# Kernel tuning notes

Hardware: AMD Instinct MI355X
Metric: run time of the kernel (lower is better)

The kernel has to match this reference:

```python
import jax, jax.numpy as jnp
import numpy as np

WS = 8           # window size
NUM_HEADS = 16
DIM = 512
HEAD_DIM = DIM // NUM_HEADS


def _relative_position_index(ws):
    coords = np.stack(np.meshgrid(np.arange(ws), np.arange(ws), indexing='ij'))  # (2, ws, ws)
    cf = coords.reshape(2, -1)                                   # (2, ws*ws)
    rel = cf[:, :, None] - cf[:, None, :]                        # (2, N, N)
    rel = rel.transpose(1, 2, 0).copy()
    rel[:, :, 0] += ws - 1
    rel[:, :, 1] += ws - 1
    rel[:, :, 0] *= 2 * ws - 1
    return jnp.asarray(rel.sum(-1))                              # (N, N) int


REL_IDX = _relative_position_index(WS)


def setup_inputs() -> dict:
    key = jax.random.key(0)
    ks = jax.random.split(key, 4)
    B, C, H, W = 4, DIM, 128, 128
    x = jax.random.normal(ks[0], (B, C, H, W), dtype=jnp.float32)
    gamma = jnp.ones((DIM,), jnp.float32)
    beta = jnp.zeros((DIM,), jnp.float32)
    w_qkv = jax.random.normal(ks[1], (DIM, 3 * DIM), jnp.float32) * (DIM ** -0.5)
    w_proj = jax.random.normal(ks[2], (DIM, DIM), jnp.float32) * (DIM ** -0.5)
    b_proj = jnp.zeros((DIM,), jnp.float32)
    bias_table = jax.random.normal(ks[3], ((2 * WS - 1) ** 2, NUM_HEADS), jnp.float32) * 0.02
    return {"x": x, "gamma": gamma, "beta": beta, "w_qkv": w_qkv,
            "w_proj": w_proj, "b_proj": b_proj, "bias_table": bias_table}


def reference(x, gamma, beta, w_qkv, w_proj, b_proj, bias_table):
    B, C, H, W = x.shape
    pad_h = (WS - H % WS) % WS
    pad_w = (WS - W % WS) % WS
    x = jnp.pad(x, ((0, 0), (0, 0), (0, pad_h), (0, pad_w)))
    Hp, Wp = H + pad_h, W + pad_w
    nh, nw = Hp // WS, Wp // WS
    N = WS * WS  # tokens per window

    # window partition: (B,C,Hp,Wp) -> (B*nh*nw, N, C)
    xw = x.reshape(B, C, nh, WS, nw, WS).transpose(0, 2, 4, 3, 5, 1)
    xw = xw.reshape(B * nh * nw, N, C)

    # LayerNorm over channels
    mu = jnp.mean(xw, axis=-1, keepdims=True)
    var = jnp.var(xw, axis=-1, keepdims=True)
    xn = (xw - mu) * jax.lax.rsqrt(var + 1e-5) * gamma + beta

    # QKV projection (no bias)
    qkv = (xn @ w_qkv).reshape(-1, N, 3, NUM_HEADS, HEAD_DIM)
    qkv = qkv.transpose(2, 0, 3, 1, 4)   # (3, nWin, heads, N, hd)
    q, k, v = qkv[0], qkv[1], qkv[2]

    scale = HEAD_DIM ** -0.5
    attn = jnp.einsum('whnd,whmd->whnm', q, k) * scale          # (nWin, heads, N, N)
    rel_bias = bias_table[REL_IDX]                               # (N, N, heads)
    attn = attn + rel_bias.transpose(2, 0, 1)[None]
    attn = jax.nn.softmax(attn, axis=-1)

    out = jnp.einsum('whnm,whmd->wnhd', attn, v).reshape(-1, N, C)
    out = out @ w_proj + b_proj

    # un-window: (B*nh*nw, N, C) -> (B, C, Hp, Wp)
    out = out.reshape(B, nh, nw, WS, WS, C).transpose(0, 5, 1, 3, 2, 4)
    out = out.reshape(B, C, Hp, Wp)
    return out[:, :, :H, :W]
```

## Files before the change

### kernel.cpp

```cpp
#include <hip/hip_runtime.h>

typedef unsigned short u16;
typedef unsigned int u32;
typedef unsigned long long u64;
typedef __bf16 bf16x8 __attribute__((ext_vector_type(8)));
typedef float f32x4 __attribute__((ext_vector_type(4)));

#define C_DIM 512
#define QKV_N 1536
#define KDIM 512
#define NHEAD 16
#define HD 32
#define H_IMG 128
#define W_IMG 128
#define HW 16384
#define NTOK 65536
#define NWIN 1024

#define GLL(g, l) __builtin_amdgcn_global_load_lds( \
    (const __attribute__((address_space(1))) u32*)(g), \
    (__attribute__((address_space(3))) u32*)(l), 16, 0, 0)

#define BAR() __builtin_amdgcn_s_barrier()
#define LGKM0() asm volatile("s_waitcnt lgkmcnt(0)" ::: "memory")
#define VM6() asm volatile("s_waitcnt vmcnt(6)" ::: "memory")
#define VM0() asm volatile("s_waitcnt vmcnt(0)" ::: "memory")

__device__ __forceinline__ u16 f2bf(float f) {
    u32 u = __builtin_bit_cast(u32, f);
    u += 0x7fffu + ((u >> 16) & 1u);
    return (u16)(u >> 16);
}
__device__ __forceinline__ float bf2f(u16 v) {
    return __builtin_bit_cast(float, (u32)v << 16);
}

__global__ void sa_prep_kernel(const float* __restrict__ w_qkv,
                               const float* __restrict__ w_proj,
                               const float* __restrict__ bias_table,
                               u16* __restrict__ wqT, u16* __restrict__ wpT,
                               u16* __restrict__ biasP) {
    int t = blockIdx.x * 256 + threadIdx.x;
    const int W1 = KDIM * QKV_N;
    const int W2 = KDIM * C_DIM;
    const int W3 = NHEAD * 64 * 64;
    if (t < W1) {
        int k = t / QKV_N, n = t % QKV_N;
        wqT[n * KDIM + k] = f2bf(w_qkv[t]);
    } else if (t < W1 + W2) {
        int u = t - W1;
        int k = u / C_DIM, n = u % C_DIM;
        wpT[n * KDIM + k] = f2bf(w_proj[u]);
    } else if (t < W1 + W2 + W3) {
        int u = t - W1 - W2;
        int h = u >> 12, n = (u >> 6) & 63, m = u & 63;
        int di = (n >> 3) - (m >> 3) + 7;
        int dj = (n & 7) - (m & 7) + 7;
        biasP[(h << 12) + (n << 6) + ((m & 15) << 2) + (m >> 4)] =
            f2bf(bias_table[(di * 15 + dj) * NHEAD + h]);
    }
}

__global__ __launch_bounds__(512, 4) void sa_ln_fused_kernel(const float* __restrict__ x,
        const float* __restrict__ gamma, const float* __restrict__ beta,
        u16* __restrict__ xnc) {
    __shared__ u16 tile[64 * 513];
    __shared__ float psum[8][64], psq[8][64];
    __shared__ float smu[64], srs[64];
    int bid = blockIdx.x;
    int win = (bid & 7) * (NWIN / 8) + (bid >> 3);
    int b = win >> 8, wl = win & 255;
    int wh = wl >> 4, ww = wl & 15;
    int tid = threadIdx.x;
    int lane = tid & 63, wv = tid >> 6;
    int cph = tid >> 4;
    int r = (tid >> 1) & 7, q = tid & 1;
    int nbase = r * 8 + q * 4;
    const float* xb = x + (size_t)b * C_DIM * HW
                        + (size_t)(wh * 8 + r) * W_IMG + ww * 8 + q * 4;
    float s[4] = {0.f, 0.f, 0.f, 0.f}, sq2[4] = {0.f, 0.f, 0.f, 0.f};
#pragma unroll
    for (int it = 0; it < 16; ++it) {
        int c = cph + it * 32;
        float4 v = *reinterpret_cast<const float4*>(xb + (size_t)c * HW);
        float vv[4] = {v.x, v.y, v.z, v.w};
#pragma unroll
        for (int e = 0; e < 4; ++e) {
            _Float16 hv = (_Float16)vv[e];
            tile[(nbase + e) * 513 + c] = __builtin_bit_cast(u16, hv);
            s[e] += vv[e]; sq2[e] += vv[e] * vv[e];
        }
    }
#pragma unroll
    for (int e = 0; e < 4; ++e) {
        s[e]   += __shfl_xor(s[e],   16, 64);  s[e]   += __shfl_xor(s[e],   32, 64);
        sq2[e] += __shfl_xor(sq2[e], 16, 64);  sq2[e] += __shfl_xor(sq2[e], 32, 64);
    }
    if ((lane >> 4) == 0) {
#pragma unroll
        for (int e = 0; e < 4; ++e) { psum[wv][nbase + e] = s[e]; psq[wv][nbase + e] = sq2[e]; }
    }
    __syncthreads();
    if (tid < 64) {
        float S = 0.f, Q = 0.f;
#pragma unroll
        for (int k = 0; k < 8; ++k) { S += psum[k][tid]; Q += psq[k][tid]; }
        float m = S * (1.f / C_DIM);
        float var = Q * (1.f / C_DIM) - m * m;
        smu[tid] = m; srs[tid] = rsqrtf(var + 1e-5f);
    }
    __syncthreads();
    int n = tid & 63;
    int gq = tid >> 6;
    float gg[8], bb[8];
#pragma unroll
    for (int c0 = 0; c0 < 8; ++c0) { gg[c0] = gamma[c0 * 64 + n]; bb[c0] = beta[c0 * 64 + n]; }
#pragma unroll
    for (int it = 0; it < 8; ++it) {
        int nn = it * 8 + gq;
        float m = smu[nn], rs = srs[nn];
        u16* op = xnc + (size_t)((win << 6) + nn) * C_DIM;
#pragma unroll
        for (int c0 = 0; c0 < 8; ++c0) {
            int c = c0 * 64 + n;
            float v = (float)__builtin_bit_cast(_Float16, tile[nn * 513 + c]);
            op[c] = f2bf((v - m) * rs * gg[c0] + bb[c0]);
        }
    }
}


#define LDA1(Q,J,KK,BUF) af[Q][J][KK] = *reinterpret_cast<const bf16x8*>( \
    &lds[(BUF)*16384 + (wr*128 + ((Q)*2+(J))*16 + lr)*64 + ((((KK)*4)+lg) ^ (lr & 7))*8])
#define LDAQ(Q,BUF) do{ LDA1(Q,0,0,BUF); LDA1(Q,0,1,BUF); LDA1(Q,1,0,BUF); LDA1(Q,1,1,BUF); }while(0)
#define LDB1(NF,KK,BUF) bfr[NF][KK] = *reinterpret_cast<const bf16x8*>( \
    &lds[32768 + (BUF)*16384 + (wc*64 + (NF)*16 + lr)*64 + ((((KK)*4)+lg) ^ (lr & 7))*8])
#define LDB(BUF) do{ LDB1(0,0,BUF); LDB1(0,1,BUF); LDB1(1,0,BUF); LDB1(1,1,BUF); \
                     LDB1(2,0,BUF); LDB1(2,1,BUF); LDB1(3,0,BUF); LDB1(3,1,BUF); }while(0)
#define MFMA1(M,N,KK) acc[M][N] = __builtin_amdgcn_mfma_f32_16x16x32_bf16(af[(M)/2][(M)&1][KK], bfr[N][KK], acc[M][N], 0, 0, 0)
#define MFMAQ(Q) do{ __builtin_amdgcn_s_setprio(1); \
    MFMA1(2*(Q),0,0);   MFMA1(2*(Q),0,1);   MFMA1(2*(Q),1,0);   MFMA1(2*(Q),1,1); \
    MFMA1(2*(Q),2,0);   MFMA1(2*(Q),2,1);   MFMA1(2*(Q),3,0);   MFMA1(2*(Q),3,1); \
    MFMA1(2*(Q)+1,0,0); MFMA1(2*(Q)+1,0,1); MFMA1(2*(Q)+1,1,0); MFMA1(2*(Q)+1,1,1); \
    MFMA1(2*(Q)+1,2,0); MFMA1(2*(Q)+1,2,1); MFMA1(2*(Q)+1,3,0); MFMA1(2*(Q)+1,3,1); \
    __builtin_amdgcn_s_setprio(0); }while(0)
#define STAGE_A(SRC, KT, H) do{ const u16* _s = (SRC) + (KT)*64 + (size_t)((H)*128)*KDIM; \
    u16* _d = Adst + ((KT)&1)*16384 + (H)*8192; \
    GLL(_s, _d); GLL(_s + (size_t)64*KDIM, _d + 4096); }while(0)
#define STAGE_B(SRC, KT, H) do{ const u16* _s = (SRC) + (KT)*64 + (size_t)((H)*128)*KDIM; \
    u16* _d = Bdst + ((KT)&1)*16384 + (H)*8192; \
    GLL(_s, _d); GLL(_s + (size_t)64*KDIM, _d + 4096); }while(0)

template <int EPI>
__device__ __forceinline__ void gemm8_body(const u16* __restrict__ A,
        const u16* __restrict__ BT, u16* __restrict__ outB, u16* __restrict__ vT,
        float* __restrict__ outF, const float* __restrict__ bias,
        int nbx, int NT, u16* lds, int nblk) {
    const int tid = threadIdx.x;
    const int lane = tid & 63, wv = tid >> 6;
    const int wr = wv >> 2, wc = wv & 3;
    const int lr = lane & 15, lg = lane >> 4;
    const int arow = tid >> 3;
    const int axs = ((tid & 7) ^ ((tid >> 3) & 7)) * 8;
    u16* Adst = lds + tid * 8;
    u16* Bdst = lds + 32768 + tid * 8;

    const int cpx = nblk >> 3;
    const int t = ((int)blockIdx.x & 7) * cpx + ((int)blockIdx.x >> 3);
    const int mb = t / nbx, nb = t % nbx;
    const int m0 = mb * 256, n0 = nb * 256;
    const u16* Asrc = A  + (size_t)(m0 + arow) * KDIM + axs;
    const u16* Bsrc = BT + (size_t)(n0 + arow) * KDIM + axs;

    bf16x8 af[4][2][2];
    bf16x8 bfr[4][2];

    STAGE_A(Asrc, 0, 0); STAGE_A(Asrc, 0, 1); STAGE_B(Bsrc, 0, 0); STAGE_B(Bsrc, 0, 1);
    STAGE_B(Bsrc, 1, 0); STAGE_B(Bsrc, 1, 1); STAGE_A(Asrc, 1, 0);
    VM6(); BAR();

    f32x4 acc[8][4];
#pragma unroll
    for (int i = 0; i < 8; ++i)
#pragma unroll
        for (int j = 0; j < 4; ++j) acc[i][j] = {0.f, 0.f, 0.f, 0.f};

#pragma unroll 1
    for (int i = 0; i < 3; ++i) {
        LDB(0); LDAQ(0, 0); STAGE_A(Asrc, 2*i + 1, 1);
        BAR(); LGKM0(); MFMAQ(0); BAR();
        LDAQ(1, 0); LDAQ(2, 0); STAGE_B(Bsrc, 2*i + 2, 0);
        BAR(); LGKM0(); MFMAQ(1); BAR();
        LDAQ(3, 0); STAGE_B(Bsrc, 2*i + 2, 1);
        BAR(); LGKM0(); MFMAQ(2); BAR();
        STAGE_A(Asrc, 2*i + 2, 0);
        BAR(); LGKM0(); MFMAQ(3); VM6(); BAR();
        LDB(1); LDAQ(0, 1); STAGE_A(Asrc, 2*i + 2, 1);
        BAR(); LGKM0(); MFMAQ(0); BAR();
        LDAQ(1, 1); LDAQ(2, 1); STAGE_B(Bsrc, 2*i + 3, 0);
        BAR(); LGKM0(); MFMAQ(1); BAR();
        LDAQ(3, 1); STAGE_B(Bsrc, 2*i + 3, 1);
        BAR(); LGKM0(); MFMAQ(2); BAR();
        STAGE_A(Asrc, 2*i + 3, 0);
        BAR(); LGKM0(); MFMAQ(3); VM6(); BAR();
    }
    LDB(0); LDAQ(0, 0); STAGE_A(Asrc, 7, 1);
    BAR(); LGKM0(); MFMAQ(0); BAR();
    LDAQ(1, 0); LDAQ(2, 0);
    BAR(); LGKM0(); MFMAQ(1); BAR();
    LDAQ(3, 0);
    BAR(); LGKM0(); MFMAQ(2); BAR();
    BAR(); LGKM0(); MFMAQ(3); VM0(); BAR();
    LDB(1); LDAQ(0, 1);
    BAR(); LGKM0(); MFMAQ(0); BAR();
    LDAQ(1, 1); LDAQ(2, 1);
    BAR(); LGKM0(); MFMAQ(1); BAR();
    LDAQ(3, 1);
    BAR(); LGKM0(); MFMAQ(2); BAR();
    BAR(); LGKM0(); MFMAQ(3);

    if (EPI == 0) {
        if (n0 < 1024) {
#pragma unroll
            for (int mf = 0; mf < 8; ++mf) {
#pragma unroll
                for (int nf = 0; nf < 4; ++nf) {
                    int col = n0 + wc * 64 + nf * 16 + lr;
                    int row = m0 + wr * 128 + mf * 16 + lg * 4;
#pragma unroll
                    for (int rr = 0; rr < 4; ++rr)
                        outB[(size_t)(row + rr) * NT + col] = f2bf(acc[mf][nf][rr]);
                }
            }
        } else {
            __syncthreads();
#pragma unroll
            for (int mf = 0; mf < 8; ++mf) {
                int row = wr * 128 + mf * 16 + lg * 4;
#pragma unroll
                for (int nf = 0; nf < 4; ++nf) {
                    int col = wc * 64 + nf * 16 + lr;
                    u64 pk = (u64)f2bf(acc[mf][nf][0])
                           | ((u64)f2bf(acc[mf][nf][1]) << 16)
                           | ((u64)f2bf(acc[mf][nf][2]) << 32)
                           | ((u64)f2bf(acc[mf][nf][3]) << 48);
                    *reinterpret_cast<u64*>(&lds[col * 256 + (row ^ ((col & 7) << 3))]) = pk;
                }
            }
            __syncthreads();
            int win0 = m0 >> 6;
#pragma unroll
            for (int j = 0; j < 16; ++j) {
                int flat = j * 512 + tid;
                int col = flat >> 5, tokc = flat & 31;
                bf16x8 v = *reinterpret_cast<const bf16x8*>(
                    &lds[col * 256 + ((tokc * 8) ^ ((col & 7) << 3))]);
                int dg = (n0 - 1024) + col;
                int head = dg >> 5, d = dg & 31;
                int win = win0 + (tokc >> 3), tok = (tokc & 7) * 8;
                *reinterpret_cast<bf16x8*>(
                    &vT[(((size_t)win * NHEAD + head) * HD + d) * 64 + tok]) = v;
            }
        }
    } else {
        int win0 = m0 >> 6;
        int b_img = win0 >> 8, wl = win0 & 255;
        int h0 = (wl >> 4) * 8, w0 = (wl & 15) * 8;
        float* fbuf = reinterpret_cast<float*>(lds);
        __syncthreads();
#pragma unroll
        for (int s = 0; s < 2; ++s) {
            if ((wc >> 1) == s) {
                int half = wc & 1;
                float* cb = fbuf + half * 16384;
#pragma unroll
                for (int mf = 0; mf < 8; ++mf) {
#pragma unroll
                    for (int nf = 0; nf < 4; ++nf) {
                        int cp = nf * 16 + lr;
                        int row = wr * 128 + mf * 16 + lg * 4;
                        int h = (row >> 3) & 7;
                        int sl = ((row >> 6) & 3) * 2 + ((row >> 2) & 1);
                        float bbv = bias[n0 + (2 * s + half) * 64 + cp];
                        f32x4 v = acc[mf][nf];
                        float4 o = {v[0] + bbv, v[1] + bbv, v[2] + bbv, v[3] + bbv};
                        *reinterpret_cast<float4*>(&cb[cp * 256 + h * 32 + (sl ^ (cp & 7)) * 4]) = o;
                    }
                }
            }
            __syncthreads();
#pragma unroll
            for (int j = 0; j < 16; ++j) {
                int flat = j * 512 + tid;
                int half = flat >> 12, f = flat & 4095;
                int cp = f >> 6, h = (f >> 3) & 7, sl = f & 7;
                int col = n0 + (2 * s + half) * 64 + cp;
                float4 v = *reinterpret_cast<const float4*>(
                    &fbuf[half * 16384 + cp * 256 + h * 32 + ((sl ^ (cp & 7))) * 4]);
                *reinterpret_cast<float4*>(outF + (size_t)(b_img * C_DIM + col) * HW
                                           + (size_t)(h0 + h) * W_IMG + w0 + sl * 4) = v;
            }
            __syncthreads();
        }
    }
}

__global__ __launch_bounds__(512, 2) void sa_qkv_gemm(const u16* __restrict__ A,
        const u16* __restrict__ BT, u16* __restrict__ outB, u16* __restrict__ vT) {
    __shared__ u16 lds[65536];
    gemm8_body<0>(A, BT, outB, vT, nullptr, nullptr, 6, QKV_N, lds, 1536);
}

__global__ __launch_bounds__(512, 2) void sa_proj_gemm(const u16* __restrict__ A,
        const u16* __restrict__ BT, float* __restrict__ outF, const float* __restrict__ bias) {
    __shared__ u16 lds[65536];
    gemm8_body<1>(A, BT, nullptr, nullptr, outF, bias, 2, C_DIM, lds, 512);
}

__global__ __launch_bounds__(64) void sa_attn_kernel(const u16* __restrict__ qkv,
        const u16* __restrict__ vT, const u16* __restrict__ biasP, u16* __restrict__ attnc) {
    __shared__ u16 Ps[64 * 72];
    int bid = blockIdx.x;
    int win  = (bid & 7) * 128 + (bid >> 7);
    int head = (bid >> 3) & 15;
    int lane = threadIdx.x, lr = lane & 15, lg = lane >> 4;
    const u16* base = qkv + (size_t)win * 64 * QKV_N + head * HD;

    bf16x8 qa[4], kb[4];
#pragma unroll
    for (int mt = 0; mt < 4; ++mt)
        qa[mt] = *reinterpret_cast<const bf16x8*>(base + (size_t)(mt * 16 + lr) * QKV_N + lg * 8);
#pragma unroll
    for (int nt = 0; nt < 4; ++nt)
        kb[nt] = *reinterpret_cast<const bf16x8*>(base + (size_t)(nt * 16 + lr) * QKV_N + 512 + lg * 8);

    f32x4 sacc[4][4];
#pragma unroll
    for (int i = 0; i < 4; ++i)
#pragma unroll
        for (int j = 0; j < 4; ++j) sacc[i][j] = {0.f, 0.f, 0.f, 0.f};
#pragma unroll
    for (int mt = 0; mt < 4; ++mt)
#pragma unroll
        for (int nt = 0; nt < 4; ++nt)
            sacc[mt][nt] = __builtin_amdgcn_mfma_f32_16x16x32_bf16(qa[mt], kb[nt], sacc[mt][nt], 0, 0, 0);

    const u16* vbase = vT + ((size_t)win * NHEAD + head) * (HD * 64);
    bf16x8 vb[2][2];
#pragma unroll
    for (int ks = 0; ks < 2; ++ks)
#pragma unroll
        for (int n2 = 0; n2 < 2; ++n2)
            vb[ks][n2] = *reinterpret_cast<const bf16x8*>(
                &vbase[(n2 * 16 + lr) * 64 + ks * 32 + lg * 8]);

    const float scale = 0.17677669529663687f;
    const u16* bp = biasP + head * 4096;
#pragma unroll
    for (int mt = 0; mt < 4; ++mt) {
#pragma unroll
        for (int rr = 0; rr < 4; ++rr) {
            int row = mt * 16 + lg * 4 + rr;
            u64 braw = *reinterpret_cast<const u64*>(&bp[row * 64 + lr * 4]);
            float vals[4];
#pragma unroll
            for (int nt = 0; nt < 4; ++nt)
                vals[nt] = sacc[mt][nt][rr] * scale + bf2f((u16)(braw >> (16 * nt)));
            float mx = fmaxf(fmaxf(vals[0], vals[1]), fmaxf(vals[2], vals[3]));
#pragma unroll
            for (int d = 1; d < 16; d <<= 1) mx = fmaxf(mx, __shfl_xor(mx, d, 64));
            float sm = 0.f;
#pragma unroll
            for (int nt = 0; nt < 4; ++nt) { vals[nt] = __expf(vals[nt] - mx); sm += vals[nt]; }
#pragma unroll
            for (int d = 1; d < 16; d <<= 1) sm += __shfl_xor(sm, d, 64);
            float inv = 1.f / sm;
#pragma unroll
            for (int nt = 0; nt < 4; ++nt)
                Ps[row * 72 + nt * 16 + lr] = f2bf(vals[nt] * inv);
        }
    }
    __syncthreads();

    f32x4 oacc[4][2];
#pragma unroll
    for (int i = 0; i < 4; ++i) { oacc[i][0] = {0.f,0.f,0.f,0.f}; oacc[i][1] = {0.f,0.f,0.f,0.f}; }
#pragma unroll
    for (int ks = 0; ks < 2; ++ks) {
        bf16x8 pa[4];
#pragma unroll
        for (int mt = 0; mt < 4; ++mt)
            pa[mt] = *reinterpret_cast<const bf16x8*>(&Ps[(mt * 16 + lr) * 72 + ks * 32 + lg * 8]);
#pragma unroll
        for (int mt = 0; mt < 4; ++mt)
#pragma unroll
            for (int n2 = 0; n2 < 2; ++n2)
                oacc[mt][n2] = __builtin_amdgcn_mfma_f32_16x16x32_bf16(pa[mt], vb[ks][n2], oacc[mt][n2], 0, 0, 0);
    }

    __syncthreads();
    u16* o_lds = Ps;
#pragma unroll
    for (int mt = 0; mt < 4; ++mt)
#pragma unroll
        for (int n2 = 0; n2 < 2; ++n2)
#pragma unroll
            for (int rr = 0; rr < 4; ++rr) {
                int row = mt * 16 + lg * 4 + rr;
                o_lds[row * 40 + n2 * 16 + lr] = f2bf(oacc[mt][n2][rr]);
            }
    __syncthreads();
    u16* ob = attnc + (size_t)win * 64 * C_DIM + head * HD;
#pragma unroll
    for (int it2 = 0; it2 < 4; ++it2) {
        int flat = it2 * 64 + lane;
        int row = flat >> 2, ch = flat & 3;
        bf16x8 v = *reinterpret_cast<const bf16x8*>(&o_lds[row * 40 + ch * 8]);
        *reinterpret_cast<bf16x8*>(&ob[(size_t)row * C_DIM + ch * 8]) = v;
    }
}

extern "C" void kernel_launch(void* const* d_in, const int* in_sizes, int n_in,
                              void* d_out, int out_size, void* d_ws, size_t ws_size,
                              hipStream_t stream) {
    const float* x          = (const float*)d_in[0];
    const float* gamma      = (const float*)d_in[1];
    const float* beta       = (const float*)d_in[2];
    const float* w_qkv      = (const float*)d_in[3];
    const float* w_proj     = (const float*)d_in[4];
    const float* b_proj     = (const float*)d_in[5];
    const float* bias_table = (const float*)d_in[6];
    float* out = (float*)d_out;

    char* ws = (char*)d_ws;
    size_t off = 0;
    auto alloc = [&](size_t bytes) {
        char* p = ws + off;
        off += (bytes + 255) & ~(size_t)255;
        return p;
    };
    u16*   wqT   = (u16*)alloc((size_t)KDIM * QKV_N * 2);
    u16*   wpT   = (u16*)alloc((size_t)KDIM * C_DIM * 2);
    u16*   biasP = (u16*)alloc((size_t)NHEAD * 64 * 64 * 2);
    u16*   xnc   = (u16*)alloc((size_t)NTOK * C_DIM * 2);
    u16*   qkvc  = (u16*)alloc((size_t)NTOK * QKV_N * 2);
    u16*   vT    = (u16*)alloc((size_t)NWIN * NHEAD * HD * 64 * 2);
    u16*   attnc = (u16*)alloc((size_t)NTOK * C_DIM * 2);

    sa_prep_kernel<<<4352, 256, 0, stream>>>(w_qkv, w_proj, bias_table, wqT, wpT, biasP);
    sa_ln_fused_kernel<<<NWIN, 512, 0, stream>>>(x, gamma, beta, xnc);
    sa_qkv_gemm<<<1536, 512, 0, stream>>>(xnc, wqT, qkvc, vT);
    sa_attn_kernel<<<NWIN * NHEAD, 64, 0, stream>>>(qkvc, vT, biasP, attnc);
    sa_proj_gemm<<<512, 512, 0, stream>>>(attnc, wpT, out, b_proj);
}
```

Measured before the change: 306.9 us.

## Fuse window attention with output projection and vectorize LayerNorm stores

Merges the per-(window,head) attention kernel and the separate projection GEMM into one kernel per window. Eight waves each handle two heads and write attention outputs into LDS, then the block does the 64x512x512 projection reading wpT directly from global and stores NCHW fp32 output. This removes the attnc intermediate round-trip and one launch. In exchange, each block rereads the full projection weight from global/L2 without LDS staging and runs a smaller, less-tiled GEMM. Separately, the LayerNorm write-back now emits 16-byte vector stores per lane with a padded tile stride.

```diff
diff --git a/kernel.cpp b/kernel.cpp
--- a/kernel.cpp
+++ b/kernel.cpp
@@ -64,7 +64,7 @@
 __global__ __launch_bounds__(512, 4) void sa_ln_fused_kernel(const float* __restrict__ x,
         const float* __restrict__ gamma, const float* __restrict__ beta,
         u16* __restrict__ xnc) {
-    __shared__ u16 tile[64 * 513];
+    __shared__ u16 tile[64 * 520];
     __shared__ float psum[8][64], psq[8][64];
     __shared__ float smu[64], srs[64];
     int bid = blockIdx.x;
@@ -87,7 +87,7 @@
 #pragma unroll
         for (int e = 0; e < 4; ++e) {
             _Float16 hv = (_Float16)vv[e];
-            tile[(nbase + e) * 513 + c] = __builtin_bit_cast(u16, hv);
+            tile[(nbase + e) * 520 + c] = __builtin_bit_cast(u16, hv);
             s[e] += vv[e]; sq2[e] += vv[e] * vv[e];
         }
     }
@@ -110,22 +110,22 @@
         smu[tid] = m; srs[tid] = rsqrtf(var + 1e-5f);
     }
     __syncthreads();
-    int n = tid & 63;
-    int gq = tid >> 6;
-    float gg[8], bb[8];
-#pragma unroll
-    for (int c0 = 0; c0 < 8; ++c0) { gg[c0] = gamma[c0 * 64 + n]; bb[c0] = beta[c0 * 64 + n]; }
+    float gg8[8], bb8[8];
+#pragma unroll
+    for (int e = 0; e < 8; ++e) { gg8[e] = gamma[lane * 8 + e]; bb8[e] = beta[lane * 8 + e]; }
 #pragma unroll
     for (int it = 0; it < 8; ++it) {
-        int nn = it * 8 + gq;
-        float m = smu[nn], rs = srs[nn];
-        u16* op = xnc + (size_t)((win << 6) + nn) * C_DIM;
-#pragma unroll
-        for (int c0 = 0; c0 < 8; ++c0) {
-            int c = c0 * 64 + n;
-            float v = (float)__builtin_bit_cast(_Float16, tile[nn * 513 + c]);
-            op[c] = f2bf((v - m) * rs * gg[c0] + bb[c0]);
-        }
+        int tok = it * 8 + wv;
+        float m = smu[tok], rs = srs[tok];
+        const u16* tp = &tile[tok * 520 + lane * 8];
+        u16 o[8];
+#pragma unroll
+        for (int e = 0; e < 8; ++e) {
+            float v = (float)__builtin_bit_cast(_Float16, tp[e]);
+            o[e] = f2bf((v - m) * rs * gg8[e] + bb8[e]);
+        }
+        *reinterpret_cast<bf16x8*>(&xnc[(size_t)((win << 6) + tok) * C_DIM + lane * 8]) =
+            *reinterpret_cast<const bf16x8*>(o);
     }
 }
 
@@ -151,11 +151,9 @@
     u16* _d = Bdst + ((KT)&1)*16384 + (H)*8192; \
     GLL(_s, _d); GLL(_s + (size_t)64*KDIM, _d + 4096); }while(0)
 
-template <int EPI>
-__device__ __forceinline__ void gemm8_body(const u16* __restrict__ A,
-        const u16* __restrict__ BT, u16* __restrict__ outB, u16* __restrict__ vT,
-        float* __restrict__ outF, const float* __restrict__ bias,
-        int nbx, int NT, u16* lds, int nblk) {
+__global__ __launch_bounds__(512, 2) void sa_qkv_gemm(const u16* __restrict__ A,
+        const u16* __restrict__ BT, u16* __restrict__ outB, u16* __restrict__ vT) {
+    __shared__ u16 lds[65536];
     const int tid = threadIdx.x;
     const int lane = tid & 63, wv = tid >> 6;
     const int wr = wv >> 2, wc = wv & 3;
@@ -165,9 +163,8 @@
     u16* Adst = lds + tid * 8;
     u16* Bdst = lds + 32768 + tid * 8;
 
-    const int cpx = nblk >> 3;
-    const int t = ((int)blockIdx.x & 7) * cpx + ((int)blockIdx.x >> 3);
-    const int mb = t / nbx, nb = t % nbx;
+    const int t = ((int)blockIdx.x & 7) * 192 + ((int)blockIdx.x >> 3);
+    const int mb = t / 6, nb = t % 6;
     const int m0 = mb * 256, n0 = nb * 256;
     const u16* Asrc = A  + (size_t)(m0 + arow) * KDIM + axs;
     const u16* Bsrc = BT + (size_t)(n0 + arow) * KDIM + axs;
@@ -219,204 +216,186 @@
     BAR(); LGKM0(); MFMAQ(2); BAR();
     BAR(); LGKM0(); MFMAQ(3);
 
-    if (EPI == 0) {
-        if (n0 < 1024) {
-#pragma unroll
-            for (int mf = 0; mf < 8; ++mf) {
-#pragma unroll
-                for (int nf = 0; nf < 4; ++nf) {
-                    int col = n0 + wc * 64 + nf * 16 + lr;
-                    int row = m0 + wr * 128 + mf * 16 + lg * 4;
-#pragma unroll
-                    for (int rr = 0; rr < 4; ++rr)
-                        outB[(size_t)(row + rr) * NT + col] = f2bf(acc[mf][nf][rr]);
-                }
+    if (n0 < 1024) {
+#pragma unroll
+        for (int mf = 0; mf < 8; ++mf) {
+#pragma unroll
+            for (int nf = 0; nf < 4; ++nf) {
+                int col = n0 + wc * 64 + nf * 16 + lr;
+                int row = m0 + wr * 128 + mf * 16 + lg * 4;
+#pragma unroll
+                for (int rr = 0; rr < 4; ++rr)
+                    outB[(size_t)(row + rr) * QKV_N + col] = f2bf(acc[mf][nf][rr]);
             }
-        } else {
-            __syncthreads();
-#pragma unroll
-            for (int mf = 0; mf < 8; ++mf) {
-                int row = wr * 128 + mf * 16 + lg * 4;
-#pragma unroll
-                for (int nf = 0; nf < 4; ++nf) {
-                    int col = wc * 64 + nf * 16 + lr;
-                    u64 pk = (u64)f2bf(acc[mf][nf][0])
-                           | ((u64)f2bf(acc[mf][nf][1]) << 16)
-                           | ((u64)f2bf(acc[mf][nf][2]) << 32)
-                           | ((u64)f2bf(acc[mf][nf][3]) << 48);
-                    *reinterpret_cast<u64*>(&lds[col * 256 + (row ^ ((col & 7) << 3))]) = pk;
-                }
+        }
+    } else {
+        __syncthreads();
+#pragma unroll
+        for (int mf = 0; mf < 8; ++mf) {
+            int row = wr * 128 + mf * 16 + lg * 4;
+#pragma unroll
+            for (int nf = 0; nf < 4; ++nf) {
+                int col = wc * 64 + nf * 16 + lr;
+                u64 pk = (u64)f2bf(acc[mf][nf][0])
+                       | ((u64)f2bf(acc[mf][nf][1]) << 16)
+                       | ((u64)f2bf(acc[mf][nf][2]) << 32)
+                       | ((u64)f2bf(acc[mf][nf][3]) << 48);
+                *reinterpret_cast<u64*>(&lds[col * 256 + (row ^ ((col & 7) << 3))]) = pk;
             }
-            __syncthreads();
-            int win0 = m0 >> 6;
-#pragma unroll
-            for (int j = 0; j < 16; ++j) {
-                int flat = j * 512 + tid;
-                int col = flat >> 5, tokc = flat & 31;
-                bf16x8 v = *reinterpret_cast<const bf16x8*>(
-                    &lds[col * 256 + ((tokc * 8) ^ ((col & 7) << 3))]);
-                int dg = (n0 - 1024) + col;
-                int head = dg >> 5, d = dg & 31;
-                int win = win0 + (tokc >> 3), tok = (tokc & 7) * 8;
-                *reinterpret_cast<bf16x8*>(
-                    &vT[(((size_t)win * NHEAD + head) * HD + d) * 64 + tok]) = v;
-            }
-        }
-    } else {
+        }
+        __syncthreads();
         int win0 = m0 >> 6;
-        int b_img = win0 >> 8, wl = win0 & 255;
-        int h0 = (wl >> 4) * 8, w0 = (wl & 15) * 8;
-        float* fbuf = reinterpret_cast<float*>(lds);
-        __syncthreads();
-#pragma unroll
-        for (int s = 0; s < 2; ++s) {
-            if ((wc >> 1) == s) {
-                int half = wc & 1;
-                float* cb = fbuf + half * 16384;
-#pragma unroll
-                for (int mf = 0; mf < 8; ++mf) {
-#pragma unroll
-                    for (int nf = 0; nf < 4; ++nf) {
-                        int cp = nf * 16 + lr;
-                        int row = wr * 128 + mf * 16 + lg * 4;
-                        int h = (row >> 3) & 7;
-                        int sl = ((row >> 6) & 3) * 2 + ((row >> 2) & 1);
-                        float bbv = bias[n0 + (2 * s + half) * 64 + cp];
-                        f32x4 v = acc[mf][nf];
-                        float4 o = {v[0] + bbv, v[1] + bbv, v[2] + bbv, v[3] + bbv};
-                        *reinterpret_cast<float4*>(&cb[cp * 256 + h * 32 + (sl ^ (cp & 7)) * 4]) = o;
-                    }
-                }
-            }
-            __syncthreads();
-#pragma unroll
-            for (int j = 0; j < 16; ++j) {
-                int flat = j * 512 + tid;
-                int half = flat >> 12, f = flat & 4095;
-                int cp = f >> 6, h = (f >> 3) & 7, sl = f & 7;
-                int col = n0 + (2 * s + half) * 64 + cp;
-                float4 v = *reinterpret_cast<const float4*>(
-                    &fbuf[half * 16384 + cp * 256 + h * 32 + ((sl ^ (cp & 7))) * 4]);
-                *reinterpret_cast<float4*>(outF + (size_t)(b_img * C_DIM + col) * HW
-                                           + (size_t)(h0 + h) * W_IMG + w0 + sl * 4) = v;
-            }
-            __syncthreads();
-        }
-    }
-}
-
-__global__ __launch_bounds__(512, 2) void sa_qkv_gemm(const u16* __restrict__ A,
-        const u16* __restrict__ BT, u16* __restrict__ outB, u16* __restrict__ vT) {
-    __shared__ u16 lds[65536];
-    gemm8_body<0>(A, BT, outB, vT, nullptr, nullptr, 6, QKV_N, lds, 1536);
-}
-
-__global__ __launch_bounds__(512, 2) void sa_proj_gemm(const u16* __restrict__ A,
-        const u16* __restrict__ BT, float* __restrict__ outF, const float* __restrict__ bias) {
-    __shared__ u16 lds[65536];
-    gemm8_body<1>(A, BT, nullptr, nullptr, outF, bias, 2, C_DIM, lds, 512);
-}
-
-__global__ __launch_bounds__(64) void sa_attn_kernel(const u16* __restrict__ qkv,
-        const u16* __restrict__ vT, const u16* __restrict__ biasP, u16* __restrict__ attnc) {
-    __shared__ u16 Ps[64 * 72];
+#pragma unroll
+        for (int j = 0; j < 16; ++j) {
+            int flat = j * 512 + tid;
+            int col = flat >> 5, tokc = flat & 31;
+            bf16x8 v = *reinterpret_cast<const bf16x8*>(
+                &lds[col * 256 + ((tokc * 8) ^ ((col & 7) << 3))]);
+            int dg = (n0 - 1024) + col;
+            int head = dg >> 5, d = dg & 31;
+            int win = win0 + (tokc >> 3), tok = (tokc & 7) * 8;
+            *reinterpret_cast<bf16x8*>(
+                &vT[(((size_t)win * NHEAD + head) * HD + d) * 64 + tok]) = v;
+        }
+    }
+}
+
+__global__ __launch_bounds__(512, 2) void sa_awp_kernel(const u16* __restrict__ qkv,
+        const u16* __restrict__ vT, const u16* __restrict__ biasP,
+        const u16* __restrict__ wpT, const float* __restrict__ b_proj,
+        float* __restrict__ out) {
+    __shared__ u16 lds[69888];
+    const int tid = threadIdx.x;
+    const int lane = tid & 63, wv = tid >> 6;
+    const int lr = lane & 15, lg = lane >> 4;
     int bid = blockIdx.x;
-    int win  = (bid & 7) * 128 + (bid >> 7);
-    int head = (bid >> 3) & 15;
-    int lane = threadIdx.x, lr = lane & 15, lg = lane >> 4;
-    const u16* base = qkv + (size_t)win * 64 * QKV_N + head * HD;
-
-    bf16x8 qa[4], kb[4];
-#pragma unroll
-    for (int mt = 0; mt < 4; ++mt)
-        qa[mt] = *reinterpret_cast<const bf16x8*>(base + (size_t)(mt * 16 + lr) * QKV_N + lg * 8);
-#pragma unroll
-    for (int nt = 0; nt < 4; ++nt)
-        kb[nt] = *reinterpret_cast<const bf16x8*>(base + (size_t)(nt * 16 + lr) * QKV_N + 512 + lg * 8);
-
-    f32x4 sacc[4][4];
-#pragma unroll
-    for (int i = 0; i < 4; ++i)
-#pragma unroll
-        for (int j = 0; j < 4; ++j) sacc[i][j] = {0.f, 0.f, 0.f, 0.f};
-#pragma unroll
-    for (int mt = 0; mt < 4; ++mt)
+    int win = (bid & 7) * 128 + (bid >> 3);
+    u16* aT = lds;
+    u16* Ps = lds + 33024 + wv * 4608;
+
+    const float scale = 0.17677669529663687f;
+#pragma unroll 1
+    for (int hi = 0; hi < 2; ++hi) {
+        int head = wv + hi * 8;
+        const u16* base = qkv + (size_t)win * 64 * QKV_N + head * HD;
+        bf16x8 qa[4], kb[4];
+#pragma unroll
+        for (int mt = 0; mt < 4; ++mt)
+            qa[mt] = *reinterpret_cast<const bf16x8*>(base + (size_t)(mt * 16 + lr) * QKV_N + lg * 8);
 #pragma unroll
         for (int nt = 0; nt < 4; ++nt)
-            sacc[mt][nt] = __builtin_amdgcn_mfma_f32_16x16x32_bf16(qa[mt], kb[nt], sacc[mt][nt], 0, 0, 0);
-
-    const u16* vbase = vT + ((size_t)win * NHEAD + head) * (HD * 64);
-    bf16x8 vb[2][2];
-#pragma unroll
-    for (int ks = 0; ks < 2; ++ks)
-#pragma unroll
-        for (int n2 = 0; n2 < 2; ++n2)
-            vb[ks][n2] = *reinterpret_cast<const bf16x8*>(
-                &vbase[(n2 * 16 + lr) * 64 + ks * 32 + lg * 8]);
-
-    const float scale = 0.17677669529663687f;
-    const u16* bp = biasP + head * 4096;
-#pragma unroll
-    for (int mt = 0; mt < 4; ++mt) {
-#pragma unroll
-        for (int rr = 0; rr < 4; ++rr) {
-            int row = mt * 16 + lg * 4 + rr;
-            u64 braw = *reinterpret_cast<const u64*>(&bp[row * 64 + lr * 4]);
-            float vals[4];
+            kb[nt] = *reinterpret_cast<const bf16x8*>(base + (size_t)(nt * 16 + lr) * QKV_N + 512 + lg * 8);
+
+        f32x4 sacc[4][4];
+#pragma unroll
+        for (int i = 0; i < 4; ++i)
+#pragma unroll
+            for (int j = 0; j < 4; ++j) sacc[i][j] = {0.f, 0.f, 0.f, 0.f};
+#pragma unroll
+        for (int mt = 0; mt < 4; ++mt)
 #pragma unroll
             for (int nt = 0; nt < 4; ++nt)
-                vals[nt] = sacc[mt][nt][rr] * scale + bf2f((u16)(braw >> (16 * nt)));
-            float mx = fmaxf(fmaxf(vals[0], vals[1]), fmaxf(vals[2], vals[3]));
-#pragma unroll
-            for (int d = 1; d < 16; d <<= 1) mx = fmaxf(mx, __shfl_xor(mx, d, 64));
-            float sm = 0.f;
-#pragma unroll
-            for (int nt = 0; nt < 4; ++nt) { vals[nt] = __expf(vals[nt] - mx); sm += vals[nt]; }
-#pragma unroll
-            for (int d = 1; d < 16; d <<= 1) sm += __shfl_xor(sm, d, 64);
-            float inv = 1.f / sm;
-#pragma unroll
-            for (int nt = 0; nt < 4; ++nt)
-                Ps[row * 72 + nt * 16 + lr] = f2bf(vals[nt] * inv);
-        }
-    }
-    __syncthreads();
-
-    f32x4 oacc[4][2];
-#pragma unroll
-    for (int i = 0; i < 4; ++i) { oacc[i][0] = {0.f,0.f,0.f,0.f}; oacc[i][1] = {0.f,0.f,0.f,0.f}; }
-#pragma unroll
-    for (int ks = 0; ks < 2; ++ks) {
-        bf16x8 pa[4];
-#pragma unroll
-        for (int mt = 0; mt < 4; ++mt)
-            pa[mt] = *reinterpret_cast<const bf16x8*>(&Ps[(mt * 16 + lr) * 72 + ks * 32 + lg * 8]);
-#pragma unroll
-        for (int mt = 0; mt < 4; ++mt)
+                sacc[mt][nt] = __builtin_amdgcn_mfma_f32_16x16x32_bf16(qa[mt], kb[nt], sacc[mt][nt], 0, 0, 0);
+
+        const u16* vbase = vT + ((size_t)win * NHEAD + head) * (HD * 64);
+        bf16x8 vb[2][2];
+#pragma unroll
+        for (int ks = 0; ks < 2; ++ks)
 #pragma unroll
             for (int n2 = 0; n2 < 2; ++n2)
-                oacc[mt][n2] = __builtin_amdgcn_mfma_f32_16x16x32_bf16(pa[mt], vb[ks][n2], oacc[mt][n2], 0, 0, 0);
-    }
-
-    __syncthreads();
-    u16* o_lds = Ps;
-#pragma unroll
-    for (int mt = 0; mt < 4; ++mt)
-#pragma unroll
-        for (int n2 = 0; n2 < 2; ++n2)
+                vb[ks][n2] = *reinterpret_cast<const bf16x8*>(
+                    &vbase[(n2 * 16 + lr) * 64 + ks * 32 + lg * 8]);
+
+        const u16* bp = biasP + head * 4096;
+#pragma unroll
+        for (int mt = 0; mt < 4; ++mt) {
 #pragma unroll
             for (int rr = 0; rr < 4; ++rr) {
                 int row = mt * 16 + lg * 4 + rr;
-                o_lds[row * 40 + n2 * 16 + lr] = f2bf(oacc[mt][n2][rr]);
+                u64 braw = *reinterpret_cast<const u64*>(&bp[row * 64 + lr * 4]);
+                float vals[4];
+#pragma unroll
+                for (int nt = 0; nt < 4; ++nt)
+                    vals[nt] = sacc[mt][nt][rr] * scale + bf2f((u16)(braw >> (16 * nt)));
+                float mx = fmaxf(fmaxf(vals[0], vals[1]), fmaxf(vals[2], vals[3]));
+#pragma unroll
+                for (int d = 1; d < 16; d <<= 1) mx = fmaxf(mx, __shfl_xor(mx, d, 64));
+                float sm = 0.f;
+#pragma unroll
+                for (int nt = 0; nt < 4; ++nt) { vals[nt] = __expf(vals[nt] - mx); sm += vals[nt]; }
+#pragma unroll
+                for (int d = 1; d < 16; d <<= 1) sm += __shfl_xor(sm, d, 64);
+                float inv = 1.f / sm;
+#pragma unroll
+                for (int nt = 0; nt < 4; ++nt)
+                    Ps[row * 72 + nt * 16 + lr] = f2bf(vals[nt] * inv);
             }
+        }
+        LGKM0();
+        __builtin_amdgcn_sched_barrier(0);
+
+        f32x4 oacc[4][2];
+#pragma unroll
+        for (int i = 0; i < 4; ++i) { oacc[i][0] = {0.f,0.f,0.f,0.f}; oacc[i][1] = {0.f,0.f,0.f,0.f}; }
+#pragma unroll
+        for (int ks = 0; ks < 2; ++ks) {
+            bf16x8 pa[4];
+#pragma unroll
+            for (int mt = 0; mt < 4; ++mt)
+                pa[mt] = *reinterpret_cast<const bf16x8*>(&Ps[(mt * 16 + lr) * 72 + ks * 32 + lg * 8]);
+#pragma unroll
+            for (int mt = 0; mt < 4; ++mt)
+#pragma unroll
+                for (int n2 = 0; n2 < 2; ++n2)
+                    oacc[mt][n2] = __builtin_amdgcn_mfma_f32_16x16x32_bf16(pa[mt], vb[ks][n2], oacc[mt][n2], 0, 0, 0);
+        }
+#pragma unroll
+        for (int mt = 0; mt < 4; ++mt)
+#pragma unroll
+            for (int n2 = 0; n2 < 2; ++n2)
+#pragma unroll
+                for (int rr = 0; rr < 4; ++rr) {
+                    int row = mt * 16 + lg * 4 + rr;
+                    aT[row * 516 + head * 32 + n2 * 16 + lr] = f2bf(oacc[mt][n2][rr]);
+                }
+    }
     __syncthreads();
-    u16* ob = attnc + (size_t)win * 64 * C_DIM + head * HD;
-#pragma unroll
-    for (int it2 = 0; it2 < 4; ++it2) {
-        int flat = it2 * 64 + lane;
-        int row = flat >> 2, ch = flat & 3;
-        bf16x8 v = *reinterpret_cast<const bf16x8*>(&o_lds[row * 40 + ch * 8]);
-        *reinterpret_cast<bf16x8*>(&ob[(size_t)row * C_DIM + ch * 8]) = v;
+
+    f32x4 pacc[4][4];
+#pragma unroll
+    for (int i = 0; i < 4; ++i)
+#pragma unroll
+        for (int j = 0; j < 4; ++j) pacc[i][j] = {0.f, 0.f, 0.f, 0.f};
+#pragma unroll
+    for (int kk = 0; kk < 16; ++kk) {
+        bf16x8 paf[4], pbf[4];
+#pragma unroll
+        for (int mt = 0; mt < 4; ++mt)
+            paf[mt] = *reinterpret_cast<const bf16x8*>(&aT[(mt * 16 + lr) * 516 + kk * 32 + lg * 8]);
+#pragma unroll
+        for (int nf = 0; nf < 4; ++nf)
+            pbf[nf] = *reinterpret_cast<const bf16x8*>(
+                &wpT[(size_t)(wv * 64 + nf * 16 + lr) * KDIM + kk * 32 + lg * 8]);
+#pragma unroll
+        for (int mt = 0; mt < 4; ++mt)
+#pragma unroll
+            for (int nf = 0; nf < 4; ++nf)
+                pacc[mt][nf] = __builtin_amdgcn_mfma_f32_16x16x32_bf16(paf[mt], pbf[nf], pacc[mt][nf], 0, 0, 0);
+    }
+    int b_img = win >> 8, wl = win & 255;
+    int h0 = (wl >> 4) * 8, w0 = (wl & 15) * 8;
+    int h = (lg >> 1), wbase = (lg & 1) * 4;
+#pragma unroll
+    for (int mt = 0; mt < 4; ++mt) {
+#pragma unroll
+        for (int nf = 0; nf < 4; ++nf) {
+            int col = wv * 64 + nf * 16 + lr;
+            float bb = b_proj[col];
+            float4 o = {pacc[mt][nf][0] + bb, pacc[mt][nf][1] + bb,
+                        pacc[mt][nf][2] + bb, pacc[mt][nf][3] + bb};
+            *reinterpret_cast<float4*>(out + (size_t)(b_img * C_DIM + col) * HW
+                + (size_t)(h0 + mt * 2 + h) * W_IMG + w0 + wbase) = o;
+        }
     }
 }
 
@@ -445,11 +424,9 @@
     u16*   xnc   = (u16*)alloc((size_t)NTOK * C_DIM * 2);
     u16*   qkvc  = (u16*)alloc((size_t)NTOK * QKV_N * 2);
     u16*   vT    = (u16*)alloc((size_t)NWIN * NHEAD * HD * 64 * 2);
-    u16*   attnc = (u16*)alloc((size_t)NTOK * C_DIM * 2);
 
     sa_prep_kernel<<<4352, 256, 0, stream>>>(w_qkv, w_proj, bias_table, wqT, wpT, biasP);
     sa_ln_fused_kernel<<<NWIN, 512, 0, stream>>>(x, gamma, beta, xnc);
     sa_qkv_gemm<<<1536, 512, 0, stream>>>(xnc, wqT, qkvc, vT);
-    sa_attn_kernel<<<NWIN * NHEAD, 64, 0, stream>>>(qkvc, vT, biasP, attnc);
-    sa_proj_gemm<<<512, 512, 0, stream>>>(attnc, wpT, out, b_proj);
-}
+    sa_awp_kernel<<<NWIN, 512, 0, stream>>>(qkvc, vT, biasP, wpT, b_proj, out);
+}
```

Result: slower. 344.9 us (+12.4%).
